# Kernel tuning notes

Hardware: AMD Instinct MI355X
Metric: run time of the kernel (lower is better)

## Reference

```python
import jax, jax.numpy as jnp
import numpy as np

B, N, DIM = 16, 1024, 512
H, KD, D = 16, 32, 128          # num_heads, key_dim, d = attn_ratio*key_dim
DH = H * D                      # 2048
HQKV = DH + 2 * H * KD          # 3072
RES = 32
SCALE = KD ** -0.5
EPS = 1e-5


def _make_bias_idxs():
    ii = np.arange(N)
    px, py = ii // RES, ii % RES
    dx = np.abs(px[:, None] - px[None, :])
    dy = np.abs(py[:, None] - py[None, :])
    return (dx * RES + dy).astype(np.int32)  # (N, N), values in [0, RES*RES)


def setup_inputs() -> dict:
    key = jax.random.key(0)
    ks = jax.random.split(key, 6)
    return {
        "x": jax.random.normal(ks[0], (B, N, DIM), jnp.float32),
        "gamma": jnp.ones((DIM,), jnp.float32),
        "beta": jnp.zeros((DIM,), jnp.float32),
        "qkv_w": jax.random.normal(ks[1], (HQKV, DIM), jnp.float32) * 0.02,
        "qkv_b": jax.random.normal(ks[2], (HQKV,), jnp.float32) * 0.02,
        "proj_w": jax.random.normal(ks[3], (DIM, DH), jnp.float32) * 0.02,
        "proj_b": jax.random.normal(ks[4], (DIM,), jnp.float32) * 0.02,
        "attention_biases": jax.random.normal(ks[5], (H, RES * RES), jnp.float32) * 0.02,
        "bias_idxs": jnp.asarray(_make_bias_idxs()),
    }


def reference(x, gamma, beta, qkv_w, qkv_b, proj_w, proj_b, attention_biases, bias_idxs):
    # LayerNorm
    mu = jnp.mean(x, axis=-1, keepdims=True)
    var = jnp.mean(jnp.square(x - mu), axis=-1, keepdims=True)
    xn = (x - mu) * jax.lax.rsqrt(var + EPS) * gamma + beta
    # QKV projection -> (B, H, N, kd+kd+d)
    qkv = (xn @ qkv_w.T + qkv_b).reshape(B, N, H, 2 * KD + D).transpose(0, 2, 1, 3)
    q, k, v = qkv[..., :KD], qkv[..., KD:2 * KD], qkv[..., 2 * KD:]
    # Relative-position bias gather: (H, N, N)
    bias = attention_biases[:, bias_idxs]
    attn = jnp.einsum("bhnk,bhmk->bhnm", q, k) * SCALE + bias
    attn = jax.nn.softmax(attn, axis=-1)
    out = jnp.einsum("bhnm,bhmd->bhnd", attn, v)  # (B, H, N, D)
    out = out.transpose(0, 2, 1, 3).reshape(B, N, DH)
    return out @ proj_w.T + proj_b
```

## Files before the change

kernel.cpp:

```cpp
#include <hip/hip_runtime.h>

#define DIM_   512
#define NSEQ   1024
#define BB     16
#define HH     16
#define KD_    32
#define DD_    128
#define LDQKV  3072
#define DH_    2048
#define SCALE_ 0.17677669529663687f

typedef __bf16 bf16x8 __attribute__((ext_vector_type(8)));
typedef float  f32x4  __attribute__((ext_vector_type(4)));

static __device__ __forceinline__ unsigned short f2bf(float f) {
  unsigned int u = __builtin_bit_cast(unsigned int, f);
  u += 0x7fffu + ((u >> 16) & 1u);
  return (unsigned short)(u >> 16);
}
#define SGM(t) ((((t) & 3) << 1) | (((t) >> 2) & 1))

__global__ __launch_bounds__(256) void cvt_kernel(const float* __restrict__ in,
                                                  unsigned short* __restrict__ out,
                                                  int n) {
  int i = blockIdx.x * 256 + threadIdx.x;
  if (i < n) out[i] = f2bf(in[i]);
}

__global__ __launch_bounds__(256) void ln_kernel(const float* __restrict__ x,
                                                 const float* __restrict__ gamma,
                                                 const float* __restrict__ beta,
                                                 unsigned short* __restrict__ xn) {
  int row = blockIdx.x, t = threadIdx.x;
  const float* xr = x + (size_t)row * DIM_;
  float2 v = *(const float2*)(xr + t * 2);
  float s = v.x + v.y, sq = v.x * v.x + v.y * v.y;
#pragma unroll
  for (int off = 32; off; off >>= 1) {
    s  += __shfl_xor(s, off, 64);
    sq += __shfl_xor(sq, off, 64);
  }
  __shared__ float red[8];
  int wid = t >> 6, lane = t & 63;
  if (lane == 0) { red[wid * 2] = s; red[wid * 2 + 1] = sq; }
  __syncthreads();
  float S  = red[0] + red[2] + red[4] + red[6];
  float SQ = red[1] + red[3] + red[5] + red[7];
  float mu   = S * (1.f / DIM_);
  float var  = SQ * (1.f / DIM_) - mu * mu;
  float rstd = rsqrtf(var + 1e-5f);
  int c = t * 2;
  xn[(size_t)row * DIM_ + c]     = f2bf((v.x - mu) * rstd * gamma[c]     + beta[c]);
  xn[(size_t)row * DIM_ + c + 1] = f2bf((v.y - mu) * rstd * gamma[c + 1] + beta[c + 1]);
}

template <typename OUT>
__global__ __launch_bounds__(256) void gemm_bf16(const unsigned short* __restrict__ A, int lda,
                                                 const unsigned short* __restrict__ W, int ldb,
                                                 const float* __restrict__ bias,
                                                 OUT* __restrict__ C, int ldc,
                                                 int K) {
  __shared__ unsigned short a_sm[128][72];
  __shared__ unsigned short b_sm[128][72];
  int tid = threadIdx.x;
  int lane = tid & 63, wid = tid >> 6;
  int quad = lane >> 4, l15 = lane & 15;
  int wr = wid >> 1, wc = wid & 1;
  long tm = (long)blockIdx.y * 128, tn = (long)blockIdx.x * 128;

  f32x4 acc[4][4] = {};

  for (int k0 = 0; k0 < K; k0 += 64) {
    __syncthreads();
#pragma unroll
    for (int i = 0; i < 4; i++) {
      int c = tid + i * 256;
      int r = c >> 3, c8 = c & 7;
      uint4 av = *(const uint4*)(A + (tm + r) * lda + k0 + c8 * 8);
      *(uint4*)&a_sm[r][c8 * 8] = av;
      uint4 bv = *(const uint4*)(W + (tn + r) * ldb + k0 + c8 * 8);
      *(uint4*)&b_sm[r][c8 * 8] = bv;
    }
    __syncthreads();
#pragma unroll
    for (int kk = 0; kk < 64; kk += 32) {
      bf16x8 af[4], bfr[4];
#pragma unroll
      for (int i = 0; i < 4; i++)
        af[i] = *(const bf16x8*)&a_sm[wr * 64 + i * 16 + l15][kk + quad * 8];
#pragma unroll
      for (int j = 0; j < 4; j++)
        bfr[j] = *(const bf16x8*)&b_sm[wc * 64 + j * 16 + l15][kk + quad * 8];
#pragma unroll
      for (int i = 0; i < 4; i++)
#pragma unroll
        for (int j = 0; j < 4; j++)
          acc[i][j] = __builtin_amdgcn_mfma_f32_16x16x32_bf16(af[i], bfr[j], acc[i][j], 0, 0, 0);
    }
  }
#pragma unroll
  for (int j = 0; j < 4; j++) {
    long col = tn + wc * 64 + j * 16 + l15;
    float bv = bias[col];
#pragma unroll
    for (int i = 0; i < 4; i++) {
      long row0 = tm + wr * 64 + i * 16 + quad * 4;
#pragma unroll
      for (int r = 0; r < 4; r++) {
        float val = acc[i][j][r] + bv;
        if constexpr (__is_same(OUT, float))
          C[(row0 + r) * ldc + col] = val;
        else
          C[(row0 + r) * ldc + col] = f2bf(val);
      }
    }
  }
}

__global__ __launch_bounds__(256) void attn_kernel(const unsigned short* __restrict__ qkv,
                                                   const float* __restrict__ ab,
                                                   unsigned short* __restrict__ attn_out) {
  __shared__ float lut[1024];
  __shared__ unsigned short vt[128][72];
  __shared__ unsigned short k_sm[64][40];
  __shared__ unsigned short p_sm[4][16][72];

  int tid = threadIdx.x;
  int lane = tid & 63, w = tid >> 6;
  int quad = lane >> 4, l15 = lane & 15;
  int qb = blockIdx.x;
  int bh = blockIdx.y;
  int b = bh >> 4, h = bh & 15;
  const unsigned short* base = qkv + (size_t)b * NSEQ * LDQKV + h * 192;

  for (int t = tid; t < 1024; t += 256) lut[t] = ab[h * 1024 + t];

  int qr = qb * 64 + w * 16 + l15;
  bf16x8 qf = *(const bf16x8*)(base + (size_t)qr * LDQKV + quad * 8);

  f32x4 accO[8] = {};
  float l_r[4] = {0.f, 0.f, 0.f, 0.f};

  int pcol_lo = (l15 & 8) | SGM(l15 & 7);
  int kkey = tid >> 2, kch = tid & 3;

  uint4 vreg[4];
  uint4 kreg;
#pragma unroll
  for (int i = 0; i < 4; i++) {
    int c = tid + i * 256;
    int m = c >> 4, c8 = c & 15;
    vreg[i] = *(const uint4*)(base + (size_t)m * LDQKV + 64 + c8 * 8);
  }
  kreg = *(const uint4*)(base + (size_t)kkey * LDQKV + 32 + kch * 8);

  for (int kt = 0; kt < 16; kt++) {
    __syncthreads();
#pragma unroll
    for (int i = 0; i < 4; i++) {
      int c = tid + i * 256;
      int m = c >> 4, c8 = c & 15;
      const unsigned short* pv = (const unsigned short*)&vreg[i];
      int col = (((m >> 3) ^ (c8 & 7)) << 3) | SGM(m & 7);
#pragma unroll
      for (int e = 0; e < 8; e++) vt[c8 * 8 + e][col] = pv[e];
    }
    *(uint4*)&k_sm[kkey][kch * 8] = kreg;
    __syncthreads();

    if (kt < 15) {
#pragma unroll
      for (int i = 0; i < 4; i++) {
        int c = tid + i * 256;
        int m = c >> 4, c8 = c & 15;
        vreg[i] = *(const uint4*)(base + (size_t)((kt + 1) * 64 + m) * LDQKV + 64 + c8 * 8);
      }
      kreg = *(const uint4*)(base + (size_t)((kt + 1) * 64 + kkey) * LDQKV + 32 + kch * 8);
    }

    f32x4 s[4];
#pragma unroll
    for (int nb = 0; nb < 4; nb++) {
      bf16x8 kf = *(const bf16x8*)&k_sm[nb * 16 + l15][quad * 8];
      f32x4 z = {};
      s[nb] = __builtin_amdgcn_mfma_f32_16x16x32_bf16(qf, kf, z, 0, 0, 0);
    }

#pragma unroll
    for (int nb = 0; nb < 4; nb++) {
      int cc = kt * 64 + nb * 16 + l15;
      int cx = cc >> 5, cy = cc & 31;
#pragma unroll
      for (int r = 0; r < 4; r++) {
        int rr = qb * 64 + w * 16 + quad * 4 + r;
        int dx = (rr >> 5) - cx; dx = dx < 0 ? -dx : dx;
        int dy = (rr & 31) - cy; dy = dy < 0 ? -dy : dy;
        float p = __expf(fmaf(s[nb][r], SCALE_, lut[dx * 32 + dy]));
        l_r[r] += p;
        p_sm[w][quad * 4 + r][nb * 16 + pcol_lo] = f2bf(p);
      }
    }
    __syncthreads();

#pragma unroll
    for (int kc = 0; kc < 2; kc++) {
      bf16x8 pf = *(const bf16x8*)&p_sm[w][l15][kc * 32 + quad * 8];
#pragma unroll
      for (int db = 0; db < 8; db++) {
        int f = (db * 2 + (l15 >> 3)) & 7;
        int colb = (((kc * 4 + quad) ^ f) << 3);
        bf16x8 vf = *(const bf16x8*)&vt[db * 16 + l15][colb];
        accO[db] = __builtin_amdgcn_mfma_f32_16x16x32_bf16(pf, vf, accO[db], 0, 0, 0);
      }
    }
  }
#pragma unroll
  for (int r = 0; r < 4; r++) {
#pragma unroll
    for (int off = 8; off; off >>= 1) l_r[r] += __shfl_xor(l_r[r], off, 16);
  }
#pragma unroll
  for (int r = 0; r < 4; r++) {
    float inv = 1.f / l_r[r];
    int row = qb * 64 + w * 16 + quad * 4 + r;
    size_t obase = ((size_t)b * NSEQ + row) * DH_ + h * DD_;
#pragma unroll
    for (int db = 0; db < 8; db++)
      attn_out[obase + db * 16 + l15] = f2bf(accO[db][r] * inv);
  }
}

extern "C" void kernel_launch(void* const* d_in, const int* in_sizes, int n_in,
                              void* d_out, int out_size, void* d_ws, size_t ws_size,
                              hipStream_t stream) {
  const float* x      = (const float*)d_in[0];
  const float* gamma  = (const float*)d_in[1];
  const float* beta   = (const float*)d_in[2];
  const float* qkv_w  = (const float*)d_in[3];
  const float* qkv_b  = (const float*)d_in[4];
  const float* proj_w = (const float*)d_in[5];
  const float* proj_b = (const float*)d_in[6];
  const float* ab     = (const float*)d_in[7];

  char* ws = (char*)d_ws;
  unsigned short* xn      = (unsigned short*)(ws);
  unsigned short* wqkv    = (unsigned short*)(ws + (size_t)16 * 1048576);
  unsigned short* wproj   = (unsigned short*)(ws + (size_t)19 * 1048576);
  unsigned short* qkv     = (unsigned short*)(ws + (size_t)21 * 1048576);
  unsigned short* attnout = (unsigned short*)(ws + (size_t)117 * 1048576);
  float* out = (float*)d_out;

  cvt_kernel<<<dim3(6144), dim3(256), 0, stream>>>(qkv_w, wqkv, 3072 * 512);
  cvt_kernel<<<dim3(4096), dim3(256), 0, stream>>>(proj_w, wproj, 512 * 2048);
  ln_kernel<<<dim3(16384), dim3(256), 0, stream>>>(x, gamma, beta, xn);
  gemm_bf16<unsigned short><<<dim3(24, 128), dim3(256), 0, stream>>>(xn, 512, wqkv, 512, qkv_b, qkv, 3072, 512);
  attn_kernel<<<dim3(16, 256), dim3(256), 0, stream>>>(qkv, ab, attnout);
  gemm_bf16<float><<<dim3(4, 128), dim3(256), 0, stream>>>(attnout, 2048, wproj, 2048, proj_b, out, 512, 2048);
}
```

Measured before the change: 449.2 us.

## Split QKV layout, pre-transpose V globally, use direct-to-LDS loads in GEMMs

The QKV GEMM now writes Q/K and V into separate compact buffers, and a new kernel pre-transposes V per head so the attention kernel loads V with plain vector stores instead of a scalar scatter transpose every tile. The GEMMs switch to global_load_lds (direct global-to-LDS) with unpadded shared tiles. The attention PV stage splits work so each wave handles two query groups and half of the D columns, sharing V fragments across two MFMAs, and the row sums are exchanged through LDS. This adds an extra kernel launch and an extra pass over V in memory, and the unpadded LDS tiles may introduce bank conflicts.

```diff
diff --git a/kernel.cpp b/kernel.cpp
--- a/kernel.cpp
+++ b/kernel.cpp
@@ -6,12 +6,15 @@
 #define HH     16
 #define KD_    32
 #define DD_    128
-#define LDQKV  3072
 #define DH_    2048
 #define SCALE_ 0.17677669529663687f
 
 typedef __bf16 bf16x8 __attribute__((ext_vector_type(8)));
 typedef float  f32x4  __attribute__((ext_vector_type(4)));
+
+typedef __attribute__((address_space(1))) const unsigned int guint;
+typedef __attribute__((address_space(3))) unsigned int luint;
+#define GLL16(gp, lp) __builtin_amdgcn_global_load_lds((guint*)(gp), (luint*)(lp), 16, 0, 0)
 
 static __device__ __forceinline__ unsigned short f2bf(float f) {
   unsigned int u = __builtin_bit_cast(unsigned int, f);
@@ -54,32 +57,28 @@
   xn[(size_t)row * DIM_ + c + 1] = f2bf((v.y - mu) * rstd * gamma[c + 1] + beta[c + 1]);
 }
 
-template <typename OUT>
-__global__ __launch_bounds__(256) void gemm_bf16(const unsigned short* __restrict__ A, int lda,
-                                                 const unsigned short* __restrict__ W, int ldb,
-                                                 const float* __restrict__ bias,
-                                                 OUT* __restrict__ C, int ldc,
-                                                 int K) {
-  __shared__ unsigned short a_sm[128][72];
-  __shared__ unsigned short b_sm[128][72];
+__global__ __launch_bounds__(256) void gemm_qkv(const unsigned short* __restrict__ A,
+                                                const unsigned short* __restrict__ W,
+                                                const float* __restrict__ bias,
+                                                unsigned short* __restrict__ qk,
+                                                unsigned short* __restrict__ vrow) {
+  __shared__ unsigned short a_sm[128][64];
+  __shared__ unsigned short b_sm[128][64];
   int tid = threadIdx.x;
-  int lane = tid & 63, wid = tid >> 6;
+  int lane = tid & 63, w = tid >> 6;
   int quad = lane >> 4, l15 = lane & 15;
-  int wr = wid >> 1, wc = wid & 1;
+  int wr = w >> 1, wc = w & 1;
   long tm = (long)blockIdx.y * 128, tn = (long)blockIdx.x * 128;
+  int srow = w * 8 + (lane >> 3), scol = (lane & 7) * 8;
 
   f32x4 acc[4][4] = {};
 
-  for (int k0 = 0; k0 < K; k0 += 64) {
-    __syncthreads();
-#pragma unroll
-    for (int i = 0; i < 4; i++) {
-      int c = tid + i * 256;
-      int r = c >> 3, c8 = c & 7;
-      uint4 av = *(const uint4*)(A + (tm + r) * lda + k0 + c8 * 8);
-      *(uint4*)&a_sm[r][c8 * 8] = av;
-      uint4 bv = *(const uint4*)(W + (tn + r) * ldb + k0 + c8 * 8);
-      *(uint4*)&b_sm[r][c8 * 8] = bv;
+  for (int k0 = 0; k0 < 512; k0 += 64) {
+    __syncthreads();
+#pragma unroll
+    for (int it = 0; it < 4; it++) {
+      GLL16(A + (tm + it * 32 + srow) * 512 + k0 + scol, &a_sm[it * 32 + w * 8][0]);
+      GLL16(W + (tn + it * 32 + srow) * 512 + k0 + scol, &b_sm[it * 32 + w * 8][0]);
     }
     __syncthreads();
 #pragma unroll
@@ -102,80 +101,152 @@
   for (int j = 0; j < 4; j++) {
     long col = tn + wc * 64 + j * 16 + l15;
     float bv = bias[col];
+    int h = (int)(col / 192), off = (int)(col - h * 192);
+    long coff = (off < 64) ? (long)h * 64 + off : (long)h * 128 + (off - 64);
+    unsigned short* dst = (off < 64) ? qk : vrow;
+    long ldo = (off < 64) ? 1024 : 2048;
 #pragma unroll
     for (int i = 0; i < 4; i++) {
       long row0 = tm + wr * 64 + i * 16 + quad * 4;
 #pragma unroll
-      for (int r = 0; r < 4; r++) {
-        float val = acc[i][j][r] + bv;
-        if constexpr (__is_same(OUT, float))
-          C[(row0 + r) * ldc + col] = val;
-        else
-          C[(row0 + r) * ldc + col] = f2bf(val);
-      }
-    }
-  }
-}
-
-__global__ __launch_bounds__(256) void attn_kernel(const unsigned short* __restrict__ qkv,
+      for (int r = 0; r < 4; r++)
+        dst[(row0 + r) * ldo + coff] = f2bf(acc[i][j][r] + bv);
+    }
+  }
+}
+
+__global__ __launch_bounds__(256) void gemm_proj(const unsigned short* __restrict__ A,
+                                                 const unsigned short* __restrict__ W,
+                                                 const float* __restrict__ bias,
+                                                 float* __restrict__ C) {
+  __shared__ unsigned short a_sm[128][64];
+  __shared__ unsigned short b_sm[128][64];
+  int tid = threadIdx.x;
+  int lane = tid & 63, w = tid >> 6;
+  int quad = lane >> 4, l15 = lane & 15;
+  int wr = w >> 1, wc = w & 1;
+  long tm = (long)blockIdx.y * 128, tn = (long)blockIdx.x * 128;
+  int srow = w * 8 + (lane >> 3), scol = (lane & 7) * 8;
+
+  f32x4 acc[4][4] = {};
+
+  for (int k0 = 0; k0 < 2048; k0 += 64) {
+    __syncthreads();
+#pragma unroll
+    for (int it = 0; it < 4; it++) {
+      GLL16(A + (tm + it * 32 + srow) * 2048 + k0 + scol, &a_sm[it * 32 + w * 8][0]);
+      GLL16(W + (tn + it * 32 + srow) * 2048 + k0 + scol, &b_sm[it * 32 + w * 8][0]);
+    }
+    __syncthreads();
+#pragma unroll
+    for (int kk = 0; kk < 64; kk += 32) {
+      bf16x8 af[4], bfr[4];
+#pragma unroll
+      for (int i = 0; i < 4; i++)
+        af[i] = *(const bf16x8*)&a_sm[wr * 64 + i * 16 + l15][kk + quad * 8];
+#pragma unroll
+      for (int j = 0; j < 4; j++)
+        bfr[j] = *(const bf16x8*)&b_sm[wc * 64 + j * 16 + l15][kk + quad * 8];
+#pragma unroll
+      for (int i = 0; i < 4; i++)
+#pragma unroll
+        for (int j = 0; j < 4; j++)
+          acc[i][j] = __builtin_amdgcn_mfma_f32_16x16x32_bf16(af[i], bfr[j], acc[i][j], 0, 0, 0);
+    }
+  }
+#pragma unroll
+  for (int j = 0; j < 4; j++) {
+    long col = tn + wc * 64 + j * 16 + l15;
+    float bv = bias[col];
+#pragma unroll
+    for (int i = 0; i < 4; i++) {
+      long row0 = tm + wr * 64 + i * 16 + quad * 4;
+#pragma unroll
+      for (int r = 0; r < 4; r++)
+        C[(row0 + r) * 512 + col] = acc[i][j][r] + bv;
+    }
+  }
+}
+
+__global__ __launch_bounds__(256) void vtrans_kernel(const unsigned short* __restrict__ vrow,
+                                                     unsigned short* __restrict__ vtg) {
+  __shared__ unsigned short vt[128][72];
+  int tid = threadIdx.x;
+  int kt = blockIdx.x, bh = blockIdx.y;
+  int b = bh >> 4, h = bh & 15;
+  const unsigned short* base = vrow + (size_t)b * NSEQ * DH_ + h * 128;
+#pragma unroll
+  for (int i = 0; i < 4; i++) {
+    int c = tid + i * 256;
+    int m = c >> 4, c8 = c & 15;
+    uint4 vv = *(const uint4*)(base + (size_t)(kt * 64 + m) * DH_ + c8 * 8);
+    const unsigned short* pv = (const unsigned short*)&vv;
+    int col = (((m >> 3) ^ (c8 & 7)) << 3) | SGM(m & 7);
+#pragma unroll
+    for (int e = 0; e < 8; e++) vt[c8 * 8 + e][col] = pv[e];
+  }
+  __syncthreads();
+#pragma unroll
+  for (int i = 0; i < 4; i++) {
+    int c = tid + i * 256;
+    int d = c >> 3, k8 = c & 7;
+    uint4 vv = *(const uint4*)&vt[d][k8 * 8];
+    *(uint4*)(vtg + ((size_t)bh * 128 + d) * NSEQ + kt * 64 + k8 * 8) = vv;
+  }
+}
+
+__global__ __launch_bounds__(256) void attn_kernel(const unsigned short* __restrict__ qk,
+                                                   const unsigned short* __restrict__ vtg,
                                                    const float* __restrict__ ab,
                                                    unsigned short* __restrict__ attn_out) {
   __shared__ float lut[1024];
   __shared__ unsigned short vt[128][72];
   __shared__ unsigned short k_sm[64][40];
   __shared__ unsigned short p_sm[4][16][72];
+  __shared__ float l_sm[64];
 
   int tid = threadIdx.x;
   int lane = tid & 63, w = tid >> 6;
   int quad = lane >> 4, l15 = lane & 15;
+  int wq = w & 1, wd = w >> 1;
   int qb = blockIdx.x;
   int bh = blockIdx.y;
   int b = bh >> 4, h = bh & 15;
-  const unsigned short* base = qkv + (size_t)b * NSEQ * LDQKV + h * 192;
+  const unsigned short* qkb = qk + (size_t)b * NSEQ * 1024 + h * 64;
+  const unsigned short* vb  = vtg + (size_t)bh * 128 * NSEQ;
 
   for (int t = tid; t < 1024; t += 256) lut[t] = ab[h * 1024 + t];
 
   int qr = qb * 64 + w * 16 + l15;
-  bf16x8 qf = *(const bf16x8*)(base + (size_t)qr * LDQKV + quad * 8);
-
-  f32x4 accO[8] = {};
+  bf16x8 qf = *(const bf16x8*)(qkb + (size_t)qr * 1024 + quad * 8);
+
+  f32x4 accO[2][4] = {};
   float l_r[4] = {0.f, 0.f, 0.f, 0.f};
 
   int pcol_lo = (l15 & 8) | SGM(l15 & 7);
   int kkey = tid >> 2, kch = tid & 3;
+  int vd = tid >> 3, vk8 = tid & 7;
 
   uint4 vreg[4];
   uint4 kreg;
 #pragma unroll
-  for (int i = 0; i < 4; i++) {
-    int c = tid + i * 256;
-    int m = c >> 4, c8 = c & 15;
-    vreg[i] = *(const uint4*)(base + (size_t)m * LDQKV + 64 + c8 * 8);
-  }
-  kreg = *(const uint4*)(base + (size_t)kkey * LDQKV + 32 + kch * 8);
+  for (int i = 0; i < 4; i++)
+    vreg[i] = *(const uint4*)(vb + (size_t)(vd + i * 32) * NSEQ + vk8 * 8);
+  kreg = *(const uint4*)(qkb + (size_t)kkey * 1024 + 32 + kch * 8);
 
   for (int kt = 0; kt < 16; kt++) {
     __syncthreads();
 #pragma unroll
-    for (int i = 0; i < 4; i++) {
-      int c = tid + i * 256;
-      int m = c >> 4, c8 = c & 15;
-      const unsigned short* pv = (const unsigned short*)&vreg[i];
-      int col = (((m >> 3) ^ (c8 & 7)) << 3) | SGM(m & 7);
-#pragma unroll
-      for (int e = 0; e < 8; e++) vt[c8 * 8 + e][col] = pv[e];
-    }
+    for (int i = 0; i < 4; i++)
+      *(uint4*)&vt[vd + i * 32][vk8 * 8] = vreg[i];
     *(uint4*)&k_sm[kkey][kch * 8] = kreg;
     __syncthreads();
 
     if (kt < 15) {
 #pragma unroll
-      for (int i = 0; i < 4; i++) {
-        int c = tid + i * 256;
-        int m = c >> 4, c8 = c & 15;
-        vreg[i] = *(const uint4*)(base + (size_t)((kt + 1) * 64 + m) * LDQKV + 64 + c8 * 8);
-      }
-      kreg = *(const uint4*)(base + (size_t)((kt + 1) * 64 + kkey) * LDQKV + 32 + kch * 8);
+      for (int i = 0; i < 4; i++)
+        vreg[i] = *(const uint4*)(vb + (size_t)(vd + i * 32) * NSEQ + (kt + 1) * 64 + vk8 * 8);
+      kreg = *(const uint4*)(qkb + (size_t)((kt + 1) * 64 + kkey) * 1024 + 32 + kch * 8);
     }
 
     f32x4 s[4];
@@ -204,13 +275,19 @@
 
 #pragma unroll
     for (int kc = 0; kc < 2; kc++) {
-      bf16x8 pf = *(const bf16x8*)&p_sm[w][l15][kc * 32 + quad * 8];
-#pragma unroll
-      for (int db = 0; db < 8; db++) {
+      bf16x8 pf[2];
+#pragma unroll
+      for (int g = 0; g < 2; g++)
+        pf[g] = *(const bf16x8*)&p_sm[wq * 2 + g][l15][kc * 32 + quad * 8];
+#pragma unroll
+      for (int j = 0; j < 4; j++) {
+        int db = wd * 4 + j;
         int f = (db * 2 + (l15 >> 3)) & 7;
-        int colb = (((kc * 4 + quad) ^ f) << 3);
+        int colb = ((kc * 4 + quad) ^ f) << 3;
         bf16x8 vf = *(const bf16x8*)&vt[db * 16 + l15][colb];
-        accO[db] = __builtin_amdgcn_mfma_f32_16x16x32_bf16(pf, vf, accO[db], 0, 0, 0);
+#pragma unroll
+        for (int g = 0; g < 2; g++)
+          accO[g][j] = __builtin_amdgcn_mfma_f32_16x16x32_bf16(pf[g], vf, accO[g][j], 0, 0, 0);
       }
     }
   }
@@ -219,14 +296,23 @@
 #pragma unroll
     for (int off = 8; off; off >>= 1) l_r[r] += __shfl_xor(l_r[r], off, 16);
   }
-#pragma unroll
-  for (int r = 0; r < 4; r++) {
-    float inv = 1.f / l_r[r];
-    int row = qb * 64 + w * 16 + quad * 4 + r;
-    size_t obase = ((size_t)b * NSEQ + row) * DH_ + h * DD_;
-#pragma unroll
-    for (int db = 0; db < 8; db++)
-      attn_out[obase + db * 16 + l15] = f2bf(accO[db][r] * inv);
+  if (l15 == 0) {
+#pragma unroll
+    for (int r = 0; r < 4; r++) l_sm[w * 16 + quad * 4 + r] = l_r[r];
+  }
+  __syncthreads();
+#pragma unroll
+  for (int g = 0; g < 2; g++) {
+#pragma unroll
+    for (int r = 0; r < 4; r++) {
+      int row16 = (wq * 2 + g) * 16 + quad * 4 + r;
+      float inv = 1.f / l_sm[row16];
+      int row = qb * 64 + row16;
+      size_t obase = ((size_t)b * NSEQ + row) * DH_ + h * DD_;
+#pragma unroll
+      for (int j = 0; j < 4; j++)
+        attn_out[obase + (wd * 4 + j) * 16 + l15] = f2bf(accO[g][j][r] * inv);
+    }
   }
 }
 
@@ -243,17 +329,20 @@
   const float* ab     = (const float*)d_in[7];
 
   char* ws = (char*)d_ws;
-  unsigned short* xn      = (unsigned short*)(ws);
-  unsigned short* wqkv    = (unsigned short*)(ws + (size_t)16 * 1048576);
-  unsigned short* wproj   = (unsigned short*)(ws + (size_t)19 * 1048576);
-  unsigned short* qkv     = (unsigned short*)(ws + (size_t)21 * 1048576);
-  unsigned short* attnout = (unsigned short*)(ws + (size_t)117 * 1048576);
+  unsigned short* xn    = (unsigned short*)(ws);
+  unsigned short* wqkv  = (unsigned short*)(ws + (size_t)16 * 1048576);
+  unsigned short* wproj = (unsigned short*)(ws + (size_t)19 * 1048576);
+  unsigned short* qkbuf = (unsigned short*)(ws + (size_t)21 * 1048576);
+  unsigned short* vrow  = (unsigned short*)(ws + (size_t)53 * 1048576);
+  unsigned short* attno = vrow;
+  unsigned short* vtg   = (unsigned short*)(ws + (size_t)117 * 1048576);
   float* out = (float*)d_out;
 
   cvt_kernel<<<dim3(6144), dim3(256), 0, stream>>>(qkv_w, wqkv, 3072 * 512);
   cvt_kernel<<<dim3(4096), dim3(256), 0, stream>>>(proj_w, wproj, 512 * 2048);
   ln_kernel<<<dim3(16384), dim3(256), 0, stream>>>(x, gamma, beta, xn);
-  gemm_bf16<unsigned short><<<dim3(24, 128), dim3(256), 0, stream>>>(xn, 512, wqkv, 512, qkv_b, qkv, 3072, 512);
-  attn_kernel<<<dim3(16, 256), dim3(256), 0, stream>>>(qkv, ab, attnout);
-  gemm_bf16<float><<<dim3(4, 128), dim3(256), 0, stream>>>(attnout, 2048, wproj, 2048, proj_b, out, 512, 2048);
-}
+  gemm_qkv<<<dim3(24, 128), dim3(256), 0, stream>>>(xn, wqkv, qkv_b, qkbuf, vrow);
+  vtrans_kernel<<<dim3(16, 256), dim3(256), 0, stream>>>(vrow, vtg);
+  attn_kernel<<<dim3(16, 256), dim3(256), 0, stream>>>(qkbuf, vtg, ab, attno);
+  gemm_proj<<<dim3(4, 128), dim3(256), 0, stream>>>(attno, wproj, proj_b, out);
+}
```

New measurement: 561.0 us. 24.9% more time.

## Use direct global-to-LDS loads in GEMM and split PV work across waves

Applied to the files above, without the earlier changes.

The GEMM tile loads now use global_load_lds 16-byte transfers straight into unpadded shared memory instead of staging through registers. In the attention kernel, each wave now computes the PV product for two query row-groups and half of the D columns, reusing each V fragment for two MFMAs and halving V LDS reads per wave. Row sums are exchanged through shared memory for the final normalisation. The unpadded 64-wide GEMM tiles may cause LDS bank conflicts on fragment reads, and the extra barrier adds a small cost.

```diff
diff --git a/kernel.cpp b/kernel.cpp
--- a/kernel.cpp
+++ b/kernel.cpp
@@ -12,6 +12,10 @@
 
 typedef __bf16 bf16x8 __attribute__((ext_vector_type(8)));
 typedef float  f32x4  __attribute__((ext_vector_type(4)));
+
+typedef __attribute__((address_space(1))) const unsigned int guint;
+typedef __attribute__((address_space(3))) unsigned int luint;
+#define GLL16(gp, lp) __builtin_amdgcn_global_load_lds((guint*)(gp), (luint*)(lp), 16, 0, 0)
 
 static __device__ __forceinline__ unsigned short f2bf(float f) {
   unsigned int u = __builtin_bit_cast(unsigned int, f);
@@ -55,31 +59,28 @@
 }
 
 template <typename OUT>
-__global__ __launch_bounds__(256) void gemm_bf16(const unsigned short* __restrict__ A, int lda,
-                                                 const unsigned short* __restrict__ W, int ldb,
-                                                 const float* __restrict__ bias,
-                                                 OUT* __restrict__ C, int ldc,
-                                                 int K) {
-  __shared__ unsigned short a_sm[128][72];
-  __shared__ unsigned short b_sm[128][72];
+__global__ __launch_bounds__(256) void gemm_gll(const unsigned short* __restrict__ A, int lda,
+                                                const unsigned short* __restrict__ W, int ldb,
+                                                const float* __restrict__ bias,
+                                                OUT* __restrict__ C, int ldc,
+                                                int K) {
+  __shared__ unsigned short a_sm[128][64];
+  __shared__ unsigned short b_sm[128][64];
   int tid = threadIdx.x;
-  int lane = tid & 63, wid = tid >> 6;
+  int lane = tid & 63, w = tid >> 6;
   int quad = lane >> 4, l15 = lane & 15;
-  int wr = wid >> 1, wc = wid & 1;
+  int wr = w >> 1, wc = w & 1;
   long tm = (long)blockIdx.y * 128, tn = (long)blockIdx.x * 128;
+  int srow = w * 8 + (lane >> 3), scol = (lane & 7) * 8;
 
   f32x4 acc[4][4] = {};
 
   for (int k0 = 0; k0 < K; k0 += 64) {
     __syncthreads();
 #pragma unroll
-    for (int i = 0; i < 4; i++) {
-      int c = tid + i * 256;
-      int r = c >> 3, c8 = c & 7;
-      uint4 av = *(const uint4*)(A + (tm + r) * lda + k0 + c8 * 8);
-      *(uint4*)&a_sm[r][c8 * 8] = av;
-      uint4 bv = *(const uint4*)(W + (tn + r) * ldb + k0 + c8 * 8);
-      *(uint4*)&b_sm[r][c8 * 8] = bv;
+    for (int it = 0; it < 4; it++) {
+      GLL16(A + (tm + it * 32 + srow) * lda + k0 + scol, &a_sm[it * 32 + w * 8][0]);
+      GLL16(W + (tn + it * 32 + srow) * ldb + k0 + scol, &b_sm[it * 32 + w * 8][0]);
     }
     __syncthreads();
 #pragma unroll
@@ -124,10 +125,12 @@
   __shared__ unsigned short vt[128][72];
   __shared__ unsigned short k_sm[64][40];
   __shared__ unsigned short p_sm[4][16][72];
+  __shared__ float l_sm[64];
 
   int tid = threadIdx.x;
   int lane = tid & 63, w = tid >> 6;
   int quad = lane >> 4, l15 = lane & 15;
+  int wq = w & 1, wd = w >> 1;
   int qb = blockIdx.x;
   int bh = blockIdx.y;
   int b = bh >> 4, h = bh & 15;
@@ -138,7 +141,7 @@
   int qr = qb * 64 + w * 16 + l15;
   bf16x8 qf = *(const bf16x8*)(base + (size_t)qr * LDQKV + quad * 8);
 
-  f32x4 accO[8] = {};
+  f32x4 accO[2][4] = {};
   float l_r[4] = {0.f, 0.f, 0.f, 0.f};
 
   int pcol_lo = (l15 & 8) | SGM(l15 & 7);
@@ -204,13 +207,19 @@
 
 #pragma unroll
     for (int kc = 0; kc < 2; kc++) {
-      bf16x8 pf = *(const bf16x8*)&p_sm[w][l15][kc * 32 + quad * 8];
-#pragma unroll
-      for (int db = 0; db < 8; db++) {
+      bf16x8 pf[2];
+#pragma unroll
+      for (int g = 0; g < 2; g++)
+        pf[g] = *(const bf16x8*)&p_sm[wq * 2 + g][l15][kc * 32 + quad * 8];
+#pragma unroll
+      for (int j = 0; j < 4; j++) {
+        int db = wd * 4 + j;
         int f = (db * 2 + (l15 >> 3)) & 7;
-        int colb = (((kc * 4 + quad) ^ f) << 3);
+        int colb = ((kc * 4 + quad) ^ f) << 3;
         bf16x8 vf = *(const bf16x8*)&vt[db * 16 + l15][colb];
-        accO[db] = __builtin_amdgcn_mfma_f32_16x16x32_bf16(pf, vf, accO[db], 0, 0, 0);
+#pragma unroll
+        for (int g = 0; g < 2; g++)
+          accO[g][j] = __builtin_amdgcn_mfma_f32_16x16x32_bf16(pf[g], vf, accO[g][j], 0, 0, 0);
       }
     }
   }
@@ -219,14 +228,23 @@
 #pragma unroll
     for (int off = 8; off; off >>= 1) l_r[r] += __shfl_xor(l_r[r], off, 16);
   }
-#pragma unroll
-  for (int r = 0; r < 4; r++) {
-    float inv = 1.f / l_r[r];
-    int row = qb * 64 + w * 16 + quad * 4 + r;
-    size_t obase = ((size_t)b * NSEQ + row) * DH_ + h * DD_;
-#pragma unroll
-    for (int db = 0; db < 8; db++)
-      attn_out[obase + db * 16 + l15] = f2bf(accO[db][r] * inv);
+  if (l15 == 0) {
+#pragma unroll
+    for (int r = 0; r < 4; r++) l_sm[w * 16 + quad * 4 + r] = l_r[r];
+  }
+  __syncthreads();
+#pragma unroll
+  for (int g = 0; g < 2; g++) {
+#pragma unroll
+    for (int r = 0; r < 4; r++) {
+      int row16 = (wq * 2 + g) * 16 + quad * 4 + r;
+      float inv = 1.f / l_sm[row16];
+      int row = qb * 64 + row16;
+      size_t obase = ((size_t)b * NSEQ + row) * DH_ + h * DD_;
+#pragma unroll
+      for (int j = 0; j < 4; j++)
+        attn_out[obase + (wd * 4 + j) * 16 + l15] = f2bf(accO[g][j][r] * inv);
+    }
   }
 }
 
@@ -253,7 +271,7 @@
   cvt_kernel<<<dim3(6144), dim3(256), 0, stream>>>(qkv_w, wqkv, 3072 * 512);
   cvt_kernel<<<dim3(4096), dim3(256), 0, stream>>>(proj_w, wproj, 512 * 2048);
   ln_kernel<<<dim3(16384), dim3(256), 0, stream>>>(x, gamma, beta, xn);
-  gemm_bf16<unsigned short><<<dim3(24, 128), dim3(256), 0, stream>>>(xn, 512, wqkv, 512, qkv_b, qkv, 3072, 512);
+  gemm_gll<unsigned short><<<dim3(24, 128), dim3(256), 0, stream>>>(xn, 512, wqkv, 512, qkv_b, qkv, 3072, 512);
   attn_kernel<<<dim3(16, 256), dim3(256), 0, stream>>>(qkv, ab, attnout);
-  gemm_bf16<float><<<dim3(4, 128), dim3(256), 0, stream>>>(attnout, 2048, wproj, 2048, proj_b, out, 512, 2048);
-}
+  gemm_gll<float><<<dim3(4, 128), dim3(256), 0, stream>>>(attnout, 2048, wproj, 2048, proj_b, out, 512, 2048);
+}
```

After: 446.1 us. Within noise of the previous version (-0.7%).
